# Kernel tuning notes

Hardware: AMD Instinct MI355X
Metric: run time of the kernel (lower is better)

Reference implementation:

```python
import jax, jax.numpy as jnp
import numpy as np

T_STEPS = 15          # SpykeTorch time dimension
THR1, THR2 = 15.0, 10.0   # conv1_threshold, conv2_threshold
KWTA2, RADIUS2 = 8, 1     # conv2_kwta, conv2_inhibition_radius


def conv2d(x, w):
    # F.conv2d, no padding, stride 1 (snn.Convolution)
    return jax.lax.conv_general_dilated(
        x, w, window_strides=(1, 1), padding='VALID',
        dimension_numbers=('NCHW', 'OIHW', 'NCHW'))


def maxpool(x, k, s):
    # sf.pooling == F.max_pool2d
    return jax.lax.reduce_window(x, -jnp.inf, jax.lax.max,
                                 (1, 1, k, k), (1, 1, s, s), 'VALID')


def fire(pot, thr):
    # sf.fire with return_thresholded_potentials=True
    pot_t = jnp.where(pot < thr, 0.0, pot)
    return jnp.sign(pot_t), pot_t


def pointwise_inhibition(pot):
    # sf.pointwise_inhibition: at each (h,w) keep only the feature that had the
    # max potential at the time of the earliest spike there.
    T, F, H, W = pot.shape
    max_vals = pot.max(axis=1, keepdims=True)            # (T,1,H,W)
    max_idx = pot.argmax(axis=1)                         # (T,H,W)
    clamp = jnp.sign(max_vals)                           # (T,1,H,W) 0/1 spike flag
    # earliest spike time per position (spikes are cumulative over T)
    earliest = jnp.clip((T - clamp.sum(axis=0)).astype(jnp.int32), 0, T - 1)  # (1,H,W)
    win_ch = jnp.take_along_axis(max_idx, earliest, axis=0)  # (1,H,W)
    # coef: one-hot over feature dim at winner channel, gated by spike at last step
    coef = (jnp.arange(F)[None, :, None, None] == win_ch[:, None, :, :]).astype(pot.dtype)
    coef = coef * clamp[-1:]                              # (1,F,H,W)
    return pot * coef


def get_k_winners(pot, spikes, kwta, radius):
    # sf.get_k_winners: rank by (earliest spike time, potential), then kwta
    # sequential suppression (same feature fully + spatial window, NMS-like).
    T, F, H, W = pot.shape
    first = jnp.clip((T - spikes.sum(axis=0, keepdims=True)).astype(jnp.int32), 0, T - 1)
    values = jnp.take_along_axis(pot, first, axis=0)      # (1,F,H,W)
    trunc = spikes * values
    v = trunc.max() * T                                   # big constant to prioritize early spikes
    total = (trunc + spikes * v).sum(axis=0)              # (F,H,W)
    fr = jnp.arange(F)[:, None, None]
    rr = jnp.arange(H)[None, :, None]
    cc = jnp.arange(W)[None, None, :]
    winners = []
    for _ in range(kwta):  # fixed small loop (kwta=8)
        idx = jnp.argmax(total)
        mx = total.reshape(-1)[idx]
        valid = mx != 0
        f = idx // (H * W)
        rem = idx % (H * W)
        r = rem // W
        c = rem % W
        winners.append(jnp.where(valid, jnp.stack([f, r, c]), -1))
        feat_hit = (fr == f)
        win_hit = (jnp.abs(rr - r) <= radius) & (jnp.abs(cc - c) <= radius)
        total = jnp.where(valid & (feat_hit | win_hit), 0.0, total)
    return jnp.stack(winners).astype(jnp.int32)           # (kwta,3)


def setup_inputs() -> dict:
    key = jax.random.key(0)
    k1, k2, k3 = jax.random.split(key, 3)
    inp = jax.random.randint(k1, (T_STEPS, 6, 160, 160), 0, 2, dtype=jnp.int32)
    # snn.Convolution weights ~ N(mean=0.8, std=0.05)
    w1 = 0.8 + 0.05 * jax.random.normal(k2, (30, 6, 5, 5), dtype=jnp.float32)
    w2 = 0.8 + 0.05 * jax.random.normal(k3, (250, 30, 3, 3), dtype=jnp.float32)
    return {"input": inp, "w1": w1, "w2": w2, "max_layer": 2}


def reference(input, w1, w2, max_layer):
    # Training-mode forward with max_layer == 2 (conv2 training branch).
    x = jnp.pad(input.astype(jnp.float32), ((0, 0), (0, 0), (2, 2), (2, 2)))
    pot = conv2d(x, w1)                                   # (15,30,160,160)
    spk, pot = fire(pot, THR1)
    spk_in = jnp.pad(maxpool(spk, 2, 2), ((0, 0), (0, 0), (1, 1), (1, 1)))
    pot = conv2d(spk_in, w2)                              # (15,250,80,80)
    spk, pot = fire(pot, THR2)
    pot = pointwise_inhibition(pot)
    spk = jnp.sign(pot)
    winners = get_k_winners(pot, spk, KWTA2, RADIUS2)
    return spk, pot, winners
```

## Files before the change

### kernel.cpp

```cpp
#include <hip/hip_runtime.h>


typedef unsigned short u16;
typedef unsigned char u8;
typedef __attribute__((ext_vector_type(8))) short short8;
typedef __attribute__((ext_vector_type(4))) float f32x4;
typedef __attribute__((ext_vector_type(4))) float float4v;

#define T_STEPS 15

#define INPCL_OFF   0u
#define SPKCL_OFF   6612480u
#define SPKROW_OFF  13067520u
#define W1CL_OFF    19119120u
#define WHI_OFF     19139600u
#define WLO_OFF     19287056u
#define MAXV_OFF    19434512u
#define ARGM_OFF    19818512u
#define WINMAP_OFF  20202512u
#define POTWIN_OFF  20228112u

#define NB_REPACK 1615
#define NB_W1     40
#define NB_W2     288
#define NB_BORD   76
#define NB_BROW   18
#define K1A_GRID  (NB_REPACK + NB_W1 + NB_W2 + NB_BORD + NB_BROW)

#define NB_CONV1  1500
#define NB_FILL   2048
#define K1B_GRID  (NB_CONV1 + NB_FILL)

static __device__ __forceinline__ u16 f2bf_rne(float f) {
  unsigned u = __float_as_uint(f);
  unsigned r = u + 0x7FFFu + ((u >> 16) & 1u);
  return (u16)(r >> 16);
}
static __device__ __forceinline__ float bf2f(u16 b) {
  return __uint_as_float(((unsigned)b) << 16);
}

__global__ __launch_bounds__(256) void prep_kernel(
    const int* __restrict__ xin, const float* __restrict__ w1,
    const float* __restrict__ w2, u16* __restrict__ inp_cl,
    u16* __restrict__ w1cl, u16* __restrict__ Whi, u16* __restrict__ Wlo,
    u16* __restrict__ spk_cl, u16* __restrict__ spk_row) {
  int tid = threadIdx.x, b = blockIdx.x;

  if (b < NB_REPACK) {
    int g = b * 256 + tid;
    if (g < 413280) {
      int t = g / 27552, rem = g % 27552;
      int yy = rem / 168, xx = rem % 168;
      int y = yy - 2, x = xx - 2;
      short8 sv = {0, 0, 0, 0, 0, 0, 0, 0};
      if ((unsigned)y < 160u && (unsigned)x < 160u) {
        const int* xb = xin + ((size_t)t * 6 * 160 + y) * 160 + x;
#pragma unroll
        for (int c = 0; c < 6; ++c)
          sv[c] = xb[c * 25600] ? (short)0x3F80 : (short)0;
      }
      *(short8*)(inp_cl + (size_t)g * 8) = sv;
    }
  } else if (b < NB_REPACK + NB_W1) {
    int idx = (b - NB_REPACK) * 256 + tid;
    int f = idx / 320, r = idx % 320;
    int ky = r / 64, r2 = r % 64;
    int kxb = r2 >> 5, k = r2 & 31;
    int dx = k >> 3, c = k & 7;
    int kx = kxb * 4 + dx;
    u16 v = 0;
    if (f < 30 && c < 6 && kx < 5)
      v = f2bf_rne(w1[(f * 6 + c) * 25 + ky * 5 + kx]);
    w1cl[idx] = v;
  } else if (b < NB_REPACK + NB_W1 + NB_W2) {
    int g2 = (b - NB_REPACK - NB_W1) * 256 + tid;
    int ks = g2 / 8192, r = g2 % 8192;
    int f = r >> 5, c = r & 31;
    u16 h = 0, l = 0;
    if (f < 250 && c < 30) {
      float w = w2[f * 270 + c * 9 + ks];
      h = f2bf_rne(w);
      l = f2bf_rne(w - bf2f(h));
    }
    Whi[g2] = h;
    Wlo[g2] = l;
  } else if (b < NB_REPACK + NB_W1 + NB_W2 + NB_BORD) {
    int u = (b - NB_REPACK - NB_W1 - NB_W2) * 256 + tid;
    if (u < 19440) {
      int pid = u >> 2, part = u & 3;
      int t = pid / 324, i = pid % 324;
      int row, col;
      if (i < 82) { row = 0; col = i; }
      else if (i < 164) { row = 81; col = i - 82; }
      else if (i < 244) { row = 1 + (i - 164); col = 0; }
      else { row = 1 + (i - 244); col = 81; }
      short8 z = {0, 0, 0, 0, 0, 0, 0, 0};
      *(short8*)(spk_cl + (((size_t)t * 82 + row) * 82 + col) * 32 +
                 part * 8) = z;
    }
  } else {
    int u0 = (b - NB_REPACK - NB_W1 - NB_W2 - NB_BORD) * 256 + tid;
    for (int v = u0; v < 145800; v += NB_BROW * 256) {
      int tc = v / 324, i = v % 324;
      int row, col;
      if (i < 82) { row = 0; col = i; }
      else if (i < 164) { row = 81; col = i - 82; }
      else if (i < 244) { row = 1 + (i - 164); col = 0; }
      else { row = 1 + (i - 244); col = 81; }
      spk_row[(size_t)tc * 6724 + row * 82 + col] = 0;
    }
  }
}

__global__ __launch_bounds__(256) void conv1_fill_kernel(
    const u16* __restrict__ inp_cl, const u16* __restrict__ w1cl,
    u16* __restrict__ spk_cl, u16* __restrict__ spk_row,
    float4v* __restrict__ out4, int out_n4) {
  __shared__ u8 fires[30 * 256];
  __shared__ u16 pooled[64 * 32];

  int tid = threadIdx.x, b = blockIdx.x;

  if (b >= NB_CONV1) {
    int i = (b - NB_CONV1) * 256 + tid;
    float4v z = {0.f, 0.f, 0.f, 0.f};
    for (; i < out_n4; i += NB_FILL * 256) out4[i] = z;
    return;
  }

  int t = b / 100, tile = b % 100;
  int ty0 = (tile / 10) * 16, tx0 = (tile % 10) * 16;
  int lane = tid & 63, wave = tid >> 6, lrow = lane & 15, lgrp = lane >> 4;

  short8 afr[2][10];
#pragma unroll
  for (int mt = 0; mt < 2; ++mt)
#pragma unroll
    for (int s = 0; s < 10; ++s)
      afr[mt][s] =
          *(const short8*)(w1cl + ((mt * 16 + lrow) * 10 + s) * 32 + lgrp * 8);

  const u16* ib = inp_cl + (size_t)t * 164 * 168 * 8;

  for (int ph = 0; ph < 4; ++ph) {
    int rrow = ph * 4 + wave;
    int oy = ty0 + rrow;
    f32x4 acc0 = {0.f, 0.f, 0.f, 0.f}, acc1 = {0.f, 0.f, 0.f, 0.f};
#pragma unroll
    for (int s = 0; s < 10; ++s) {
      int ky = s >> 1, kxb = s & 1;
      short8 bfr = *(const short8*)(
          ib + (((oy + ky) * 168) + tx0 + lrow + kxb * 4 + lgrp) * 8);
      acc0 = __builtin_amdgcn_mfma_f32_16x16x32_bf16(afr[0][s], bfr, acc0,
                                                     0, 0, 0);
      acc1 = __builtin_amdgcn_mfma_f32_16x16x32_bf16(afr[1][s], bfr, acc1,
                                                     0, 0, 0);
    }
#pragma unroll
    for (int r = 0; r < 4; ++r) {
      int f0 = lgrp * 4 + r;
      fires[f0 * 256 + rrow * 16 + lrow] = (acc0[r] >= 15.f);
      int f1 = 16 + lgrp * 4 + r;
      if (f1 < 30) fires[f1 * 256 + rrow * 16 + lrow] = (acc1[r] >= 15.f);
    }
  }
  __syncthreads();

  int pby0 = (ty0 >> 1) + 1, pbx0 = (tx0 >> 1) + 1;

  for (int idx = tid; idx < 2048; idx += 256) {
    int f = idx >> 6, pp = idx & 63;
    int py = pp >> 3, px = pp & 7;
    u16 v = 0;
    if (f < 30) {
      const u8* fb = &fires[f * 256 + py * 32 + px * 2];
      v = (fb[0] | fb[1] | fb[16] | fb[17]) ? (u16)0x3F80 : (u16)0;
    }
    pooled[pp * 32 + f] = v;
  }
  for (int idx = tid; idx < 1920; idx += 256) {
    int f = idx >> 6, pp = idx & 63;
    int py = pp >> 3, px = pp & 7;
    const u8* fb = &fires[f * 256 + py * 32 + px * 2];
    u16 v = (fb[0] | fb[1] | fb[16] | fb[17]) ? (u16)0x3F80 : (u16)0;
    spk_row[((t * 30 + f) * 82 + pby0 + py) * 82 + pbx0 + px] = v;
  }
  __syncthreads();

  int pos = tid >> 2, part = tid & 3;
  int yy = pby0 + (pos >> 3), xx = pbx0 + (pos & 7);
  *(short8*)(spk_cl + (((size_t)t * 82 + yy) * 82 + xx) * 32 + part * 8) =
      *(short8*)&pooled[pos * 32 + part * 8];
}

__global__ __launch_bounds__(512) void conv2_kernel(
    const u16* __restrict__ spk_cl, const u16* __restrict__ Whi,
    const u16* __restrict__ Wlo, float* __restrict__ maxv_ws,
    int* __restrict__ argm_ws) {
  __shared__ float redv[64 * 9];
  __shared__ int redi[64 * 9];

  int tid = threadIdx.x, b = blockIdx.x;
  int t = b / 100, tile = b % 100;
  int x0 = (tile % 5) * 16, y0 = (tile / 5) * 4;
  int lane = tid & 63, wave = tid >> 6, lrow = lane & 15, lgrp = lane >> 4;
  int fbase = wave * 32;

  f32x4 acc[2][4];
#pragma unroll
  for (int i = 0; i < 2; ++i)
#pragma unroll
    for (int j = 0; j < 4; ++j) acc[i][j] = (f32x4){0.f, 0.f, 0.f, 0.f};

  const u16* sb = spk_cl + (size_t)t * 82 * 82 * 32;
  const u16* whb = Whi + (fbase + lrow) * 32 + lgrp * 8;
  const u16* wlb = Wlo + (fbase + lrow) * 32 + lgrp * 8;

  short8 ah[2][2], al[2][2], bfv[2][4];
#pragma unroll
  for (int ft = 0; ft < 2; ++ft) {
    ah[0][ft] = *(const short8*)(whb + ft * 512);
    al[0][ft] = *(const short8*)(wlb + ft * 512);
  }
#pragma unroll
  for (int pt = 0; pt < 4; ++pt)
    bfv[0][pt] =
        *(const short8*)(sb + (((y0 + pt) * 82) + x0 + lrow) * 32 + lgrp * 8);

#pragma unroll
  for (int ks = 0; ks < 9; ++ks) {
    int cur = ks & 1, nxt = cur ^ 1;
    if (ks < 8) {
      int kn = ks + 1;
      int kyn = kn / 3, kxn = kn % 3;
#pragma unroll
      for (int ft = 0; ft < 2; ++ft) {
        ah[nxt][ft] = *(const short8*)(whb + kn * 8192 + ft * 512);
        al[nxt][ft] = *(const short8*)(wlb + kn * 8192 + ft * 512);
      }
#pragma unroll
      for (int pt = 0; pt < 4; ++pt)
        bfv[nxt][pt] = *(const short8*)(
            sb + (((y0 + pt + kyn) * 82) + x0 + lrow + kxn) * 32 + lgrp * 8);
    }
#pragma unroll
    for (int ft = 0; ft < 2; ++ft)
#pragma unroll
      for (int pt = 0; pt < 4; ++pt) {
        acc[ft][pt] = __builtin_amdgcn_mfma_f32_16x16x32_bf16(
            ah[cur][ft], bfv[cur][pt], acc[ft][pt], 0, 0, 0);
        acc[ft][pt] = __builtin_amdgcn_mfma_f32_16x16x32_bf16(
            al[cur][ft], bfv[cur][pt], acc[ft][pt], 0, 0, 0);
      }
  }

#pragma unroll
  for (int pt = 0; pt < 4; ++pt) {
    float bv = -1.f; int bf = 0;
#pragma unroll
    for (int ft = 0; ft < 2; ++ft)
#pragma unroll
      for (int r = 0; r < 4; ++r) {
        float v = acc[ft][pt][r];
        v = (v >= 10.f) ? v : 0.f;
        int f = fbase + ft * 16 + lgrp * 4 + r;
        if (v > bv) { bv = v; bf = f; }
      }
    {
      float ov = __shfl_xor(bv, 16); int of = __shfl_xor(bf, 16);
      if (ov > bv || (ov == bv && of < bf)) { bv = ov; bf = of; }
      ov = __shfl_xor(bv, 32); of = __shfl_xor(bf, 32);
      if (ov > bv || (ov == bv && of < bf)) { bv = ov; bf = of; }
    }
    if (lgrp == 0) {
      int p = pt * 16 + lrow;
      redv[p * 9 + wave] = bv;
      redi[p * 9 + wave] = bf;
    }
  }
  __syncthreads();
  if (tid < 64) {
    float bv = -1.f; int bf = 0x7fffffff;
#pragma unroll
    for (int w = 0; w < 8; ++w) {
      float v = redv[tid * 9 + w]; int f = redi[tid * 9 + w];
      if (v > bv || (v == bv && f < bf)) { bv = v; bf = f; }
    }
    int y = y0 + (tid >> 4), x = x0 + (tid & 15);
    int pos = y * 80 + x;
    maxv_ws[t * 6400 + pos] = bv;
    argm_ws[t * 6400 + pos] = bf;
  }
}

__global__ __launch_bounds__(256) void recompute_kernel(
    const u16* __restrict__ spk_row, const float* __restrict__ w2,
    const float* __restrict__ maxv, const int* __restrict__ argm,
    int* __restrict__ winmap, float* __restrict__ potwin) {
  __shared__ u16 patch[30 * 18 * 18];

  int tid = threadIdx.x, b = blockIdx.x;
  int t = b / 25, tile = b % 25;
  int ty0 = (tile / 5) * 16, tx0 = (tile % 5) * 16;

  const u16* base = spk_row + (size_t)t * 30 * 6724;
  unsigned* p32 = (unsigned*)patch;
  for (int idx = tid; idx < 4860; idx += 256) {
    int c = idx / 162, rem = idx % 162;
    int dy = rem / 9, dxp = rem % 9;
    p32[idx] = *(const unsigned*)(base + c * 6724 + (ty0 + dy) * 82 + tx0 +
                                  dxp * 2);
  }

  int py = tid >> 4, px = tid & 15;
  int pos = (ty0 + py) * 80 + tx0 + px;

  int nc = 0;
#pragma unroll
  for (int tt = 0; tt < T_STEPS; ++tt)
    nc += (maxv[tt * 6400 + pos] > 0.f) ? 1 : 0;
  int e = T_STEPS - nc; if (e > 14) e = 14;
  int win = argm[e * 6400 + pos];
  if (!(maxv[14 * 6400 + pos] > 0.f)) win = -1;
  if (t == 0) winmap[pos] = win;

  __syncthreads();

  float p = 0.f;
  if (win >= 0) {
    const float* wt = w2 + win * 270;
    float a = 0.f;
    for (int c = 0; c < 30; ++c) {
#pragma unroll
      for (int ky = 0; ky < 3; ++ky)
#pragma unroll
        for (int kx = 0; kx < 3; ++kx)
          a = fmaf(wt[c * 9 + ky * 3 + kx],
                   bf2f(patch[c * 324 + (py + ky) * 18 + (px + kx)]), a);
    }
    p = (a >= 10.f) ? a : 0.f;
  }
  potwin[t * 6400 + pos] = p;
}

__global__ __launch_bounds__(1024) void finalize_kernel(
    const int* __restrict__ winmap, const float* __restrict__ potwin,
    float* __restrict__ out, float* __restrict__ out_win) {
  __shared__ float tv[6400];
  __shared__ int   tf[6400];
  __shared__ float wv_s[16];
  __shared__ int   wk_s[16];
  __shared__ int   sh_w[4];
  __shared__ float vmax_s;

  int tid = threadIdx.x;
  int b = blockIdx.x;

  if (b > 0) {
    int pos = (b - 1) * 256 + (tid & 255);
    int tq = tid >> 8;
    int win = winmap[pos];
    if (win < 0) return;
    int tend = tq * 4 + 4; if (tend > T_STEPS) tend = T_STEPS;
    for (int t = tq * 4; t < tend; ++t) {
      float p = potwin[t * 6400 + pos];
      int o = (t * 250 + win) * 6400 + pos;
      out[o] = (p > 0.f) ? 1.f : 0.f;
      out[24000000 + o] = p;
    }
    return;
  }

  int lane = tid & 63, wid = tid >> 6;

  float localmax = 0.f;
  for (int pos = tid; pos < 6400; pos += 1024) {
    int win = winmap[pos];
    float val = 0.f; int nspk = 0;
    if (win >= 0) {
#pragma unroll
      for (int t = 0; t < T_STEPS; ++t)
        nspk += (potwin[t * 6400 + pos] > 0.f) ? 1 : 0;
      int first = T_STEPS - nspk; if (first > 14) first = 14;
      val = potwin[first * 6400 + pos];
      if (nspk > 0 && val > localmax) localmax = val;
    }
    tv[pos] = val;
    tf[pos] = ((win + 1) << 4) | nspk;
  }
#pragma unroll
  for (int m = 1; m < 64; m <<= 1)
    localmax = fmaxf(localmax, __shfl_xor(localmax, m));
  if (lane == 0) wv_s[wid] = localmax;
  __syncthreads();
  if (tid == 0) {
    float m = 0.f;
#pragma unroll
    for (int w = 0; w < 16; ++w) m = fmaxf(m, wv_s[w]);
    vmax_s = m * (float)T_STEPS;
  }
  __syncthreads();
  float v = vmax_s;

  for (int pos = tid; pos < 6400; pos += 1024) {
    int meta = tf[pos];
    int win = (meta >> 4) - 1, nspk = meta & 15;
    tf[pos] = win;
    tv[pos] = (win >= 0) ? (float)nspk * (tv[pos] + v) : 0.f;
  }
  __syncthreads();

  for (int it = 0; it < 8; ++it) {
    float bv = -1.f; int bk = 0x7fffffff;
    for (int pos = tid; pos < 6400; pos += 1024) {
      float tvv = tv[pos];
      int key = tf[pos] * 6400 + pos;
      if (tvv > bv || (tvv == bv && key < bk)) { bv = tvv; bk = key; }
    }
#pragma unroll
    for (int m = 1; m < 64; m <<= 1) {
      float ov = __shfl_xor(bv, m); int ok = __shfl_xor(bk, m);
      if (ov > bv || (ov == bv && ok < bk)) { bv = ov; bk = ok; }
    }
    if (lane == 0) { wv_s[wid] = bv; wk_s[wid] = bk; }
    __syncthreads();
    if (tid == 0) {
      float mbv = -1.f; int mbk = 0x7fffffff;
#pragma unroll
      for (int w = 0; w < 16; ++w) {
        float ov = wv_s[w]; int ok = wk_s[w];
        if (ov > mbv || (ov == mbv && ok < mbk)) { mbv = ov; mbk = ok; }
      }
      int f = -1, r = -1, c = -1, valid = 0;
      if (mbv != 0.f) {
        f = mbk / 6400; int pos = mbk % 6400;
        r = pos / 80; c = pos % 80;
        valid = 1;
      }
      out_win[it * 3 + 0] = (float)f;
      out_win[it * 3 + 1] = (float)r;
      out_win[it * 3 + 2] = (float)c;
      sh_w[0] = f; sh_w[1] = r; sh_w[2] = c; sh_w[3] = valid;
    }
    __syncthreads();
    if (sh_w[3]) {
      int wf = sh_w[0], wr = sh_w[1], wc = sh_w[2];
      for (int pos = tid; pos < 6400; pos += 1024) {
        int r = pos / 80, c = pos % 80;
        int dr = r - wr; if (dr < 0) dr = -dr;
        int dc = c - wc; if (dc < 0) dc = -dc;
        if (tf[pos] == wf || (dr <= 1 && dc <= 1)) tv[pos] = 0.f;
      }
    }
    __syncthreads();
  }
}

extern "C" void kernel_launch(void* const* d_in, const int* in_sizes, int n_in,
                              void* d_out, int out_size, void* d_ws,
                              size_t ws_size, hipStream_t stream) {
  const int*   xin = (const int*)d_in[0];
  const float* w1  = (const float*)d_in[1];
  const float* w2  = (const float*)d_in[2];
  float* out = (float*)d_out;
  char*  ws  = (char*)d_ws;

  u16*   inp_cl  = (u16*)(ws + INPCL_OFF);
  u16*   spk_cl  = (u16*)(ws + SPKCL_OFF);
  u16*   spk_row = (u16*)(ws + SPKROW_OFF);
  u16*   w1cl    = (u16*)(ws + W1CL_OFF);
  u16*   Whi     = (u16*)(ws + WHI_OFF);
  u16*   Wlo     = (u16*)(ws + WLO_OFF);
  float* maxv    = (float*)(ws + MAXV_OFF);
  int*   argm    = (int*)(ws + ARGM_OFF);
  int*   winmap  = (int*)(ws + WINMAP_OFF);
  float* potwin  = (float*)(ws + POTWIN_OFF);

  prep_kernel<<<K1A_GRID, 256, 0, stream>>>(xin, w1, w2, inp_cl, w1cl, Whi,
                                            Wlo, spk_cl, spk_row);
  conv1_fill_kernel<<<K1B_GRID, 256, 0, stream>>>(inp_cl, w1cl, spk_cl,
                                                  spk_row, (float4v*)d_out,
                                                  out_size / 4);
  conv2_kernel<<<1500, 512, 0, stream>>>(spk_cl, Whi, Wlo, maxv, argm);
  recompute_kernel<<<375, 256, 0, stream>>>(spk_row, w2, maxv, argm, winmap,
                                            potwin);
  finalize_kernel<<<26, 1024, 0, stream>>>(winmap, potwin, out,
                                           out + 48000000);
}
```

Before: 152.0 us.

## Process two time steps per conv2 block and move output zero-fill into conv2

Each conv2 block now computes two consecutive time steps, so every loaded weight fragment feeds both timesteps' MFMAs and weight traffic per output is halved. The zero-fill of the large output buffer moves from the conv1 launch into the conv2 launch, so the memory-bound fill can overlap the MFMA-heavy conv2 instead of the conv1 work. The software prefetch of spike fragments is dropped in favour of per-step loads, and launch bounds request 3 blocks per CU. Risks are higher register pressure from doubled accumulators, less latency hiding on the B loads, and wasted work on the odd last timestep.

```diff
diff --git a/kernel.cpp b/kernel.cpp
--- a/kernel.cpp
+++ b/kernel.cpp
@@ -28,8 +28,10 @@
 #define K1A_GRID  (NB_REPACK + NB_W1 + NB_W2 + NB_BORD + NB_BROW)
 
 #define NB_CONV1  1500
-#define NB_FILL   2048
-#define K1B_GRID  (NB_CONV1 + NB_FILL)
+
+#define NB_CONV2  800
+#define NB_FILL2  2048
+#define K2_GRID   (NB_CONV2 + NB_FILL2)
 
 static __device__ __forceinline__ u16 f2bf_rne(float f) {
   unsigned u = __float_as_uint(f);
@@ -113,22 +115,13 @@
   }
 }
 
-__global__ __launch_bounds__(256) void conv1_fill_kernel(
+__global__ __launch_bounds__(256) void conv1_kernel(
     const u16* __restrict__ inp_cl, const u16* __restrict__ w1cl,
-    u16* __restrict__ spk_cl, u16* __restrict__ spk_row,
-    float4v* __restrict__ out4, int out_n4) {
+    u16* __restrict__ spk_cl, u16* __restrict__ spk_row) {
   __shared__ u8 fires[30 * 256];
   __shared__ u16 pooled[64 * 32];
 
   int tid = threadIdx.x, b = blockIdx.x;
-
-  if (b >= NB_CONV1) {
-    int i = (b - NB_CONV1) * 256 + tid;
-    float4v z = {0.f, 0.f, 0.f, 0.f};
-    for (; i < out_n4; i += NB_FILL * 256) out4[i] = z;
-    return;
-  }
-
   int t = b / 100, tile = b % 100;
   int ty0 = (tile / 10) * 16, tx0 = (tile % 10) * 16;
   int lane = tid & 63, wave = tid >> 6, lrow = lane & 15, lgrp = lane >> 4;
@@ -194,103 +187,122 @@
       *(short8*)&pooled[pos * 32 + part * 8];
 }
 
-__global__ __launch_bounds__(512) void conv2_kernel(
+__global__ __launch_bounds__(512, 3) void conv2_fill_kernel(
     const u16* __restrict__ spk_cl, const u16* __restrict__ Whi,
     const u16* __restrict__ Wlo, float* __restrict__ maxv_ws,
-    int* __restrict__ argm_ws) {
+    int* __restrict__ argm_ws, float4v* __restrict__ out4, int out_n4) {
   __shared__ float redv[64 * 9];
   __shared__ int redi[64 * 9];
 
   int tid = threadIdx.x, b = blockIdx.x;
-  int t = b / 100, tile = b % 100;
+
+  if (b >= NB_CONV2) {
+    int i = (b - NB_CONV2) * 512 + tid;
+    float4v z = {0.f, 0.f, 0.f, 0.f};
+    for (; i < out_n4; i += NB_FILL2 * 512) out4[i] = z;
+    return;
+  }
+
+  int tp = b / 100, tile = b % 100;
+  int t0 = tp * 2;
+  bool has_t1 = (t0 + 1) < T_STEPS;
   int x0 = (tile % 5) * 16, y0 = (tile / 5) * 4;
   int lane = tid & 63, wave = tid >> 6, lrow = lane & 15, lgrp = lane >> 4;
   int fbase = wave * 32;
 
-  f32x4 acc[2][4];
-#pragma unroll
-  for (int i = 0; i < 2; ++i)
-#pragma unroll
-    for (int j = 0; j < 4; ++j) acc[i][j] = (f32x4){0.f, 0.f, 0.f, 0.f};
-
-  const u16* sb = spk_cl + (size_t)t * 82 * 82 * 32;
+  f32x4 acc[2][2][4];
+#pragma unroll
+  for (int tt = 0; tt < 2; ++tt)
+#pragma unroll
+    for (int i = 0; i < 2; ++i)
+#pragma unroll
+      for (int j = 0; j < 4; ++j) acc[tt][i][j] = (f32x4){0.f, 0.f, 0.f, 0.f};
+
+  const u16* sb0 = spk_cl + (size_t)t0 * 215168;
+  const u16* sb1 = has_t1 ? (sb0 + 215168) : sb0;
   const u16* whb = Whi + (fbase + lrow) * 32 + lgrp * 8;
   const u16* wlb = Wlo + (fbase + lrow) * 32 + lgrp * 8;
 
-  short8 ah[2][2], al[2][2], bfv[2][4];
+  short8 ah[2][2], al[2][2];
 #pragma unroll
   for (int ft = 0; ft < 2; ++ft) {
     ah[0][ft] = *(const short8*)(whb + ft * 512);
     al[0][ft] = *(const short8*)(wlb + ft * 512);
   }
-#pragma unroll
-  for (int pt = 0; pt < 4; ++pt)
-    bfv[0][pt] =
-        *(const short8*)(sb + (((y0 + pt) * 82) + x0 + lrow) * 32 + lgrp * 8);
 
 #pragma unroll
   for (int ks = 0; ks < 9; ++ks) {
     int cur = ks & 1, nxt = cur ^ 1;
+    int ky = ks / 3, kx = ks % 3;
     if (ks < 8) {
       int kn = ks + 1;
-      int kyn = kn / 3, kxn = kn % 3;
 #pragma unroll
       for (int ft = 0; ft < 2; ++ft) {
         ah[nxt][ft] = *(const short8*)(whb + kn * 8192 + ft * 512);
         al[nxt][ft] = *(const short8*)(wlb + kn * 8192 + ft * 512);
       }
-#pragma unroll
-      for (int pt = 0; pt < 4; ++pt)
-        bfv[nxt][pt] = *(const short8*)(
-            sb + (((y0 + pt + kyn) * 82) + x0 + lrow + kxn) * 32 + lgrp * 8);
+    }
+    short8 b0[4], b1[4];
+#pragma unroll
+    for (int pt = 0; pt < 4; ++pt) {
+      size_t off = (((y0 + pt + ky) * 82) + x0 + lrow + kx) * 32 + lgrp * 8;
+      b0[pt] = *(const short8*)(sb0 + off);
+      b1[pt] = *(const short8*)(sb1 + off);
     }
 #pragma unroll
     for (int ft = 0; ft < 2; ++ft)
 #pragma unroll
       for (int pt = 0; pt < 4; ++pt) {
-        acc[ft][pt] = __builtin_amdgcn_mfma_f32_16x16x32_bf16(
-            ah[cur][ft], bfv[cur][pt], acc[ft][pt], 0, 0, 0);
-        acc[ft][pt] = __builtin_amdgcn_mfma_f32_16x16x32_bf16(
-            al[cur][ft], bfv[cur][pt], acc[ft][pt], 0, 0, 0);
-      }
-  }
-
-#pragma unroll
-  for (int pt = 0; pt < 4; ++pt) {
-    float bv = -1.f; int bf = 0;
-#pragma unroll
-    for (int ft = 0; ft < 2; ++ft)
-#pragma unroll
-      for (int r = 0; r < 4; ++r) {
-        float v = acc[ft][pt][r];
-        v = (v >= 10.f) ? v : 0.f;
-        int f = fbase + ft * 16 + lgrp * 4 + r;
-        if (v > bv) { bv = v; bf = f; }
-      }
-    {
-      float ov = __shfl_xor(bv, 16); int of = __shfl_xor(bf, 16);
-      if (ov > bv || (ov == bv && of < bf)) { bv = ov; bf = of; }
-      ov = __shfl_xor(bv, 32); of = __shfl_xor(bf, 32);
-      if (ov > bv || (ov == bv && of < bf)) { bv = ov; bf = of; }
-    }
-    if (lgrp == 0) {
-      int p = pt * 16 + lrow;
-      redv[p * 9 + wave] = bv;
-      redi[p * 9 + wave] = bf;
-    }
-  }
-  __syncthreads();
-  if (tid < 64) {
-    float bv = -1.f; int bf = 0x7fffffff;
-#pragma unroll
-    for (int w = 0; w < 8; ++w) {
-      float v = redv[tid * 9 + w]; int f = redi[tid * 9 + w];
-      if (v > bv || (v == bv && f < bf)) { bv = v; bf = f; }
-    }
-    int y = y0 + (tid >> 4), x = x0 + (tid & 15);
-    int pos = y * 80 + x;
-    maxv_ws[t * 6400 + pos] = bv;
-    argm_ws[t * 6400 + pos] = bf;
+        acc[0][ft][pt] = __builtin_amdgcn_mfma_f32_16x16x32_bf16(
+            ah[cur][ft], b0[pt], acc[0][ft][pt], 0, 0, 0);
+        acc[0][ft][pt] = __builtin_amdgcn_mfma_f32_16x16x32_bf16(
+            al[cur][ft], b0[pt], acc[0][ft][pt], 0, 0, 0);
+        acc[1][ft][pt] = __builtin_amdgcn_mfma_f32_16x16x32_bf16(
+            ah[cur][ft], b1[pt], acc[1][ft][pt], 0, 0, 0);
+        acc[1][ft][pt] = __builtin_amdgcn_mfma_f32_16x16x32_bf16(
+            al[cur][ft], b1[pt], acc[1][ft][pt], 0, 0, 0);
+      }
+  }
+
+  for (int tt = 0; tt < 2; ++tt) {
+#pragma unroll
+    for (int pt = 0; pt < 4; ++pt) {
+      float bv = -1.f; int bf = 0;
+#pragma unroll
+      for (int ft = 0; ft < 2; ++ft)
+#pragma unroll
+        for (int r = 0; r < 4; ++r) {
+          float v = acc[tt][ft][pt][r];
+          v = (v >= 10.f) ? v : 0.f;
+          int f = fbase + ft * 16 + lgrp * 4 + r;
+          if (v > bv) { bv = v; bf = f; }
+        }
+      {
+        float ov = __shfl_xor(bv, 16); int of = __shfl_xor(bf, 16);
+        if (ov > bv || (ov == bv && of < bf)) { bv = ov; bf = of; }
+        ov = __shfl_xor(bv, 32); of = __shfl_xor(bf, 32);
+        if (ov > bv || (ov == bv && of < bf)) { bv = ov; bf = of; }
+      }
+      if (lgrp == 0) {
+        int p = pt * 16 + lrow;
+        redv[p * 9 + wave] = bv;
+        redi[p * 9 + wave] = bf;
+      }
+    }
+    __syncthreads();
+    if (tid < 64 && (tt == 0 || has_t1)) {
+      float bv = -1.f; int bf = 0x7fffffff;
+#pragma unroll
+      for (int w = 0; w < 8; ++w) {
+        float v = redv[tid * 9 + w]; int f = redi[tid * 9 + w];
+        if (v > bv || (v == bv && f < bf)) { bv = v; bf = f; }
+      }
+      int y = y0 + (tid >> 4), x = x0 + (tid & 15);
+      int pos = y * 80 + x;
+      maxv_ws[(t0 + tt) * 6400 + pos] = bv;
+      argm_ws[(t0 + tt) * 6400 + pos] = bf;
+    }
+    __syncthreads();
   }
 }
 
@@ -479,10 +491,10 @@
 
   prep_kernel<<<K1A_GRID, 256, 0, stream>>>(xin, w1, w2, inp_cl, w1cl, Whi,
                                             Wlo, spk_cl, spk_row);
-  conv1_fill_kernel<<<K1B_GRID, 256, 0, stream>>>(inp_cl, w1cl, spk_cl,
-                                                  spk_row, (float4v*)d_out,
-                                                  out_size / 4);
-  conv2_kernel<<<1500, 512, 0, stream>>>(spk_cl, Whi, Wlo, maxv, argm);
+  conv1_kernel<<<NB_CONV1, 256, 0, stream>>>(inp_cl, w1cl, spk_cl, spk_row);
+  conv2_fill_kernel<<<K2_GRID, 512, 0, stream>>>(spk_cl, Whi, Wlo, maxv,
+                                                 argm, (float4v*)d_out,
+                                                 out_size / 4);
   recompute_kernel<<<375, 256, 0, stream>>>(spk_row, w2, maxv, argm, winmap,
                                             potwin);
   finalize_kernel<<<26, 1024, 0, stream>>>(winmap, potwin, out,
```

Result: slower. 159.8 us (+5.1%).
